# Kernel tuning notes

Measured on AMD Instinct MI355X. Metric: run time of the kernel, lower is better.

## Reference

```python
import jax, jax.numpy as jnp
import numpy as np

EMBED_DIM = 1024
NUM_HEADS = 16
HEAD_DIM = EMBED_DIM // NUM_HEADS


def setup_inputs() -> dict:
    key = jax.random.key(0)
    k1, k2, k3, k4 = jax.random.split(key, 4)
    S, B = 2048, 2
    x = jax.random.normal(k1, (S, B, EMBED_DIM), dtype=jnp.float32)
    # xavier_uniform for in_proj_weight [3E, E]
    limit_in = float(np.sqrt(6.0 / (3 * EMBED_DIM + EMBED_DIM)))
    in_proj_weight = jax.random.uniform(k2, (3 * EMBED_DIM, EMBED_DIM), minval=-limit_in, maxval=limit_in, dtype=jnp.float32)
    in_proj_bias = jnp.zeros((3 * EMBED_DIM,), dtype=jnp.float32)
    # out_proj: nn.Linear default init (kaiming-uniform-ish); use uniform of similar scale
    limit_out = float(np.sqrt(1.0 / EMBED_DIM))
    out_proj_weight = jax.random.uniform(k3, (EMBED_DIM, EMBED_DIM), minval=-limit_out, maxval=limit_out, dtype=jnp.float32)
    out_proj_bias = jnp.zeros((EMBED_DIM,), dtype=jnp.float32)
    return {
        "x": x,
        "in_proj_weight": in_proj_weight,
        "in_proj_bias": in_proj_bias,
        "out_proj_weight": out_proj_weight,
        "out_proj_bias": out_proj_bias,
    }


def reference(x, in_proj_weight, in_proj_bias, out_proj_weight, out_proj_bias):
    S, B, E = x.shape
    H, D = NUM_HEADS, HEAD_DIM
    scaling = float(D) ** -0.5
    # fused QKV projection: [S, B, 3E]
    qkv = jnp.einsum("sbe,fe->sbf", x, in_proj_weight) + in_proj_bias
    q, k, v = jnp.split(qkv, 3, axis=-1)
    q = q * scaling
    # [S, B, E] -> [B*H, S, D]
    def to_heads(t):
        return t.reshape(S, B * H, D).transpose(1, 0, 2)
    q, k, v = to_heads(q), to_heads(k), to_heads(v)
    # attention scores [B*H, S, S]
    scores = jnp.einsum("btd,bsd->bts", q, k)
    weights = jax.nn.softmax(scores, axis=-1)
    # dropout p=0.0 -> identity
    attn = jnp.einsum("bts,bsd->btd", weights, v)  # [B*H, S, D]
    attn = attn.transpose(1, 0, 2).reshape(S, B, E)
    out = jnp.einsum("sbe,fe->sbf", attn, out_proj_weight) + out_proj_bias
    return out
```

## Files before the change

### kernel.cpp

```cpp
#include <hip/hip_runtime.h>

typedef __bf16 bf16_t;
typedef __attribute__((ext_vector_type(8))) __bf16 bf16x8;
typedef __attribute__((ext_vector_type(4))) __bf16 bf16x4;
typedef __attribute__((ext_vector_type(4))) float f32x4;
typedef __attribute__((ext_vector_type(16))) float f32x16;
typedef __attribute__((ext_vector_type(2))) unsigned uint2v;

#define MFMA16(a, b, c) __builtin_amdgcn_mfma_f32_16x16x32_bf16((a), (b), (c), 0, 0, 0)
#define MFMA32(a, b, c) __builtin_amdgcn_mfma_f32_32x32x16_bf16((a), (b), (c), 0, 0, 0)
#define LOG2E 1.44269504088896f

__device__ __forceinline__ void async16(const bf16_t* g, bf16_t* l) {
    __builtin_amdgcn_global_load_lds(
        (const __attribute__((address_space(1))) unsigned int*)g,
        (__attribute__((address_space(3))) unsigned int*)l, 16, 0, 0);
}

__device__ __forceinline__ unsigned pack2(float a, float b) {
    union { bf16_t e[2]; unsigned u; } x;
    x.e[0] = (bf16_t)a; x.e[1] = (bf16_t)b;
    return x.u;
}

__device__ __forceinline__ void pl32swap(unsigned& a, unsigned& b) {
    uint2v r = __builtin_amdgcn_permlane32_swap(a, b, false, false);
    a = r[0]; b = r[1];
}

__global__ __launch_bounds__(256) void conv3(
    const float* __restrict__ s0, const float* __restrict__ s1,
    const float* __restrict__ s2, bf16_t* __restrict__ dst,
    int n0, int n1)
{
    const int i = (blockIdx.x * 256 + threadIdx.x) * 8;
    const float* src;
    int off;
    if (i < n0)           { src = s0; off = 0; }
    else if (i < n0 + n1) { src = s1; off = n0; }
    else                  { src = s2; off = n0 + n1; }
    const float4 a = *reinterpret_cast<const float4*>(src + i - off);
    const float4 b = *reinterpret_cast<const float4*>(src + i - off + 4);
    bf16x8 o;
    o[0] = (bf16_t)a.x; o[1] = (bf16_t)a.y; o[2] = (bf16_t)a.z; o[3] = (bf16_t)a.w;
    o[4] = (bf16_t)b.x; o[5] = (bf16_t)b.y; o[6] = (bf16_t)b.z; o[7] = (bf16_t)b.w;
    *reinterpret_cast<bf16x8*>(dst + i) = o;
}

__global__ __launch_bounds__(256) void vtrans(
    const bf16_t* __restrict__ qkv, bf16_t* __restrict__ vT, int B)
{
    const int bh = blockIdx.x, b = bh >> 4, h = bh & 15;
    const int s0 = blockIdx.y * 64;
    __shared__ bf16_t Ls[64][65];
    const int t = threadIdx.x;
    const int sl = t & 63, dc = t >> 6;
#pragma unroll
    for (int pass = 0; pass < 2; pass++) {
        const int d8 = dc + pass * 4;
        bf16x8 v = *reinterpret_cast<const bf16x8*>(
            qkv + (size_t)((s0 + sl) * B + b) * 3072 + 2048 + h * 64 + d8 * 8);
#pragma unroll
        for (int j = 0; j < 8; j++) Ls[sl][d8 * 8 + j] = v[j];
    }
    __syncthreads();
#pragma unroll
    for (int pass = 0; pass < 2; pass++) {
        const int cid = t + pass * 256;
        const int d = cid >> 3, cs = cid & 7;
        bf16x8 o;
#pragma unroll
        for (int j = 0; j < 8; j++) o[j] = Ls[cs * 8 + j][d];
        *reinterpret_cast<bf16x8*>(
            vT + (size_t)(bh * 64 + d) * 2048 + s0 + cs * 8) = o;
    }
}

template <int MT, bool F32OUT>
__global__ __launch_bounds__(256, 3) void gemm_nt_lds(
    const bf16_t* __restrict__ W, const bf16_t* __restrict__ X,
    const float* __restrict__ bias, void* __restrict__ Cv,
    int N, int K, int scale_lim, float qscale, int fpx)
{
    constexpr int NJ = MT / 32;
    __shared__ bf16_t As[2][128 * 32];
    __shared__ bf16_t Bs[2][MT * 32];

    const int lane = threadIdx.x & 63;
    const int wv   = threadIdx.x >> 6;
    const int l15  = lane & 15;
    const int qd   = lane >> 4;

    const int id = blockIdx.x;
    const int x8 = id & 7, k = id >> 3;
    const int fb = ((k % fpx) * 8 + x8) * 128;
    const int mb = (k / fpx) * MT;
    const int fw = (wv & 1) * 64;
    const int mw = (wv >> 1) * (MT / 2);

    f32x4 acc[4][NJ] = {};

    auto stage = [&](int set, int k0) {
#pragma unroll
        for (int t = 0; t < 2; t++) {
            const int p = (wv * 2 + t) * 64 + lane;
            const int r = p >> 2, cl = (p & 3) ^ (r & 3);
            async16(W + (size_t)(fb + r) * K + k0 + cl * 8,
                    &As[set][(wv * 2 + t) * 512]);
        }
#pragma unroll
        for (int t = 0; t < MT / 64; t++) {
            const int p = (wv * (MT / 64) + t) * 64 + lane;
            const int r = p >> 2, cl = (p & 3) ^ (r & 3);
            async16(X + (size_t)(mb + r) * K + k0 + cl * 8,
                    &Bs[set][(wv * (MT / 64) + t) * 512]);
        }
    };

    stage(0, 0);
    int set = 0;
    for (int k0 = 0; k0 < K; k0 += 32) {
        __syncthreads();
        if (k0 + 32 < K) stage(set ^ 1, k0 + 32);

        const int s3 = l15 & 3;
        bf16x8 a[4], bb[NJ];
#pragma unroll
        for (int i = 0; i < 4; i++)
            a[i] = *reinterpret_cast<const bf16x8*>(
                &As[set][(fw + i * 16 + l15) * 32 + ((qd ^ s3) * 8)]);
#pragma unroll
        for (int j = 0; j < NJ; j++)
            bb[j] = *reinterpret_cast<const bf16x8*>(
                &Bs[set][(mw + j * 16 + l15) * 32 + ((qd ^ s3) * 8)]);
#pragma unroll
        for (int i = 0; i < 4; i++)
#pragma unroll
            for (int j = 0; j < NJ; j++)
                acc[i][j] = MFMA16(a[i], bb[j], acc[i][j]);
        set ^= 1;
    }

    const float scale = (fb < scale_lim) ? qscale : 1.0f;
#pragma unroll
    for (int i = 0; i < 4; i++) {
        const int f0 = fb + fw + i * 16 + qd * 4;
        float bs[4];
#pragma unroll
        for (int r = 0; r < 4; r++) bs[r] = bias[f0 + r];
#pragma unroll
        for (int j = 0; j < NJ; j++) {
            const int m = mb + mw + j * 16 + l15;
            if (F32OUT) {
                float4 o;
                o.x = (acc[i][j][0] + bs[0]) * scale;
                o.y = (acc[i][j][1] + bs[1]) * scale;
                o.z = (acc[i][j][2] + bs[2]) * scale;
                o.w = (acc[i][j][3] + bs[3]) * scale;
                *reinterpret_cast<float4*>((float*)Cv + (size_t)m * N + f0) = o;
            } else {
                bf16x4 o;
#pragma unroll
                for (int r = 0; r < 4; r++)
                    o[r] = (bf16_t)((acc[i][j][r] + bs[r]) * scale);
                *reinterpret_cast<bf16x4*>((bf16_t*)Cv + (size_t)m * N + f0) = o;
            }
        }
    }
}

__global__ __launch_bounds__(256, 2) void flash_attn(
    const bf16_t* __restrict__ qkv, const bf16_t* __restrict__ vT,
    bf16_t* __restrict__ attn, int S, int B)
{
    const int E3 = 3072, E = 1024;
    const int bh = blockIdx.x, b = bh >> 4, h = bh & 15;
    const int tid = threadIdx.x, lane = tid & 63, wv = tid >> 6;
    const int qw = wv & 1;
    const int pr = wv >> 1;
    const int l31 = lane & 31, half = lane >> 5;

    __shared__ bf16_t Kt[2][2][64 * 64];
    __shared__ bf16_t Vt[2][2][64 * 64];
    __shared__ float  lsh[2][64];

    const int q0 = blockIdx.y * 128 + qw * 64;

    bf16x8 qf[2][4];
#pragma unroll
    for (int qt = 0; qt < 2; qt++) {
        const bf16_t* qp = qkv + (size_t)((q0 + qt * 32 + l31) * B + b) * E3 + h * 64;
#pragma unroll
        for (int ks = 0; ks < 4; ks++)
            qf[qt][ks] = *reinterpret_cast<const bf16x8*>(qp + ks * 16 + half * 8);
    }

    f32x16 oacc[2][2] = {};
    float lrun[2] = {0.0f, 0.0f};

    auto stage = [&](int set, int kv) {
#pragma unroll
        for (int t = 0; t < 4; t++) {
            const int p = (qw * 4 + t) * 64 + lane;
            const int r = p >> 3, cl = (p & 7) ^ (r & 7);
            async16(qkv + (size_t)((kv + r) * B + b) * E3 + E + h * 64 + cl * 8,
                    &Kt[pr][set][(qw * 4 + t) * 512]);
            async16(vT + (size_t)(bh * 64 + r) * 2048 + kv + cl * 8,
                    &Vt[pr][set][(qw * 4 + t) * 512]);
        }
    };

    const int kvbase = pr * (S / 2);
    const int NIT = S / 128;

    stage(0, kvbase);
    int set = 0;
    for (int it = 0; it < NIT; it++) {
        __syncthreads();
        if (it + 1 < NIT) stage(set ^ 1, kvbase + (it + 1) * 64);

        const bf16_t* K_ = Kt[pr][set];
        const bf16_t* V_ = Vt[pr][set];

        union PF { unsigned u[4]; bf16x8 v; };
        PF pf[2][4];
#pragma unroll
        for (int nt = 0; nt < 2; nt++) {
            const int r = nt * 32 + l31;
            const int r7 = r & 7;
            bf16x8 kf[4];
#pragma unroll
            for (int ks = 0; ks < 4; ks++)
                kf[ks] = *reinterpret_cast<const bf16x8*>(
                    K_ + r * 64 + (((ks * 2 + half) ^ r7) * 8));
#pragma unroll
            for (int qt = 0; qt < 2; qt++) {
                f32x16 st = {};
                __builtin_amdgcn_s_setprio(1);
#pragma unroll
                for (int ks = 0; ks < 4; ks++)
                    st = MFMA32(kf[ks], qf[qt][ks], st);
                __builtin_amdgcn_s_setprio(0);
                float ls = 0.0f;
                unsigned q8[8];
#pragma unroll
                for (int g = 0; g < 4; g++) {
                    const float p0 = __builtin_amdgcn_exp2f(st[4 * g]);
                    const float p1 = __builtin_amdgcn_exp2f(st[4 * g + 1]);
                    const float p2 = __builtin_amdgcn_exp2f(st[4 * g + 2]);
                    const float p3 = __builtin_amdgcn_exp2f(st[4 * g + 3]);
                    ls += (p0 + p1) + (p2 + p3);
                    q8[2 * g]     = pack2(p0, p1);
                    q8[2 * g + 1] = pack2(p2, p3);
                }
                lrun[qt] += ls;
                pl32swap(q8[0], q8[2]); pl32swap(q8[1], q8[3]);
                pl32swap(q8[4], q8[6]); pl32swap(q8[5], q8[7]);
                pf[qt][nt * 2 + 0].u[0] = q8[0]; pf[qt][nt * 2 + 0].u[1] = q8[1];
                pf[qt][nt * 2 + 0].u[2] = q8[2]; pf[qt][nt * 2 + 0].u[3] = q8[3];
                pf[qt][nt * 2 + 1].u[0] = q8[4]; pf[qt][nt * 2 + 1].u[1] = q8[5];
                pf[qt][nt * 2 + 1].u[2] = q8[6]; pf[qt][nt * 2 + 1].u[3] = q8[7];
            }
        }
        __builtin_amdgcn_s_setprio(1);
#pragma unroll
        for (int kn = 0; kn < 4; kn++)
#pragma unroll
            for (int dt = 0; dt < 2; dt++) {
                const int d = dt * 32 + l31;
                bf16x8 vf = *reinterpret_cast<const bf16x8*>(
                    V_ + d * 64 + (((kn * 2 + half) ^ (d & 7)) * 8));
                oacc[0][dt] = MFMA32(vf, pf[0][kn].v, oacc[0][dt]);
                oacc[1][dt] = MFMA32(vf, pf[1][kn].v, oacc[1][dt]);
            }
        __builtin_amdgcn_s_setprio(0);
        set ^= 1;
    }

    __syncthreads();
    float lr[2];
#pragma unroll
    for (int qt = 0; qt < 2; qt++) lr[qt] = lrun[qt] + __shfl_xor(lrun[qt], 32);

    float* fo = reinterpret_cast<float*>(&Kt[0][0][0]) + qw * 4096;

    if (pr == 1) {
#pragma unroll
        for (int qt = 0; qt < 2; qt++) {
            const int ql = qt * 32 + l31;
            lsh[qw][ql] = lr[qt];
#pragma unroll
            for (int dt = 0; dt < 2; dt++)
#pragma unroll
                for (int g = 0; g < 4; g++)
#pragma unroll
                    for (int r = 0; r < 4; r++) {
                        const int d = dt * 32 + g * 8 + half * 4 + r;
                        fo[d * 64 + ql] = oacc[qt][dt][4 * g + r];
                    }
        }
    }
    __syncthreads();
    if (pr == 0) {
#pragma unroll
        for (int qt = 0; qt < 2; qt++) {
            const int ql = qt * 32 + l31;
            const float inv = 1.0f / (lr[qt] + lsh[qw][ql]);
            const int qrow = q0 + qt * 32 + l31;
#pragma unroll
            for (int dt = 0; dt < 2; dt++)
#pragma unroll
                for (int g = 0; g < 4; g++) {
                    bf16x4 o;
#pragma unroll
                    for (int r = 0; r < 4; r++) {
                        const int d = dt * 32 + g * 8 + half * 4 + r;
                        o[r] = (bf16_t)((oacc[qt][dt][4 * g + r] + fo[d * 64 + ql]) * inv);
                    }
                    *reinterpret_cast<bf16x4*>(attn + (size_t)(qrow * B + b) * E +
                                               h * 64 + dt * 32 + g * 8 + half * 4) = o;
                }
        }
    }
}

extern "C" void kernel_launch(void* const* d_in, const int* in_sizes, int n_in,
                              void* d_out, int out_size, void* d_ws, size_t ws_size,
                              hipStream_t stream) {
    const float* x  = (const float*)d_in[0];
    const float* wi = (const float*)d_in[1];
    const float* bi = (const float*)d_in[2];
    const float* wo = (const float*)d_in[3];
    const float* bo = (const float*)d_in[4];
    float* out = (float*)d_out;

    const int S = 2048, B = 2, E = 1024;
    const int M = S * B;

    bf16_t* xb   = (bf16_t*)d_ws;
    bf16_t* wib  = xb  + (size_t)M * E;
    bf16_t* wob  = wib + (size_t)3 * E * E;
    bf16_t* qkv  = wob + (size_t)E * E;
    bf16_t* attn = qkv + (size_t)M * 3 * E;
    bf16_t* vT   = xb;

    const int n0 = M * E, n1 = 3 * E * E, n2 = E * E;
    conv3<<<(n0 + n1 + n2) / 8 / 256, 256, 0, stream>>>(x, wi, wo, xb, n0, n1);

    gemm_nt_lds<128, false><<<(3 * E / 128) * (M / 128), 256, 0, stream>>>(
        wib, xb, bi, qkv, 3 * E, E, E, 0.125f * LOG2E, (3 * E / 128) / 8);

    vtrans<<<dim3(B * 16, S / 64), 256, 0, stream>>>(qkv, vT, B);

    flash_attn<<<dim3(B * 16, S / 128), 256, 0, stream>>>(qkv, vT, attn, S, B);

    gemm_nt_lds<64, true><<<(E / 128) * (M / 64), 256, 0, stream>>>(
        wob, attn, bo, out, E, E, 0, 1.0f, (E / 128) / 8);
}
```

Measured before the change: 194.1 us.

## Software-pipeline attention loop, overlapping previous tile's PV MFMAs with current QK softmax

Restructures the flash-attention inner loop so the P·V product for the previous KV tile is interleaved with the Q·K MFMAs and exp2 softmax of the current tile. P fragments are double-buffered in registers (pfA/pfB), and V staging is delayed by one iteration with its own buffer indexing. A final epilogue does the last tile's PV after the loop. The aim is to hide exp/pack latency behind MFMA work, at the cost of higher register pressure and more complex buffer indexing.

```diff
diff --git a/kernel.cpp b/kernel.cpp
--- a/kernel.cpp
+++ b/kernel.cpp
@@ -198,32 +198,30 @@
     f32x16 oacc[2][2] = {};
     float lrun[2] = {0.0f, 0.0f};
 
-    auto stage = [&](int set, int kv) {
+    auto stageK = [&](int kset, int kv) {
 #pragma unroll
         for (int t = 0; t < 4; t++) {
             const int p = (qw * 4 + t) * 64 + lane;
             const int r = p >> 3, cl = (p & 7) ^ (r & 7);
             async16(qkv + (size_t)((kv + r) * B + b) * E3 + E + h * 64 + cl * 8,
-                    &Kt[pr][set][(qw * 4 + t) * 512]);
+                    &Kt[pr][kset][(qw * 4 + t) * 512]);
+        }
+    };
+    auto stageV = [&](int vset, int kv) {
+#pragma unroll
+        for (int t = 0; t < 4; t++) {
+            const int p = (qw * 4 + t) * 64 + lane;
+            const int r = p >> 3, cl = (p & 7) ^ (r & 7);
             async16(vT + (size_t)(bh * 64 + r) * 2048 + kv + cl * 8,
-                    &Vt[pr][set][(qw * 4 + t) * 512]);
+                    &Vt[pr][vset][(qw * 4 + t) * 512]);
         }
     };
 
-    const int kvbase = pr * (S / 2);
-    const int NIT = S / 128;
-
-    stage(0, kvbase);
-    int set = 0;
-    for (int it = 0; it < NIT; it++) {
-        __syncthreads();
-        if (it + 1 < NIT) stage(set ^ 1, kvbase + (it + 1) * 64);
-
-        const bf16_t* K_ = Kt[pr][set];
-        const bf16_t* V_ = Vt[pr][set];
-
-        union PF { unsigned u[4]; bf16x8 v; };
-        PF pf[2][4];
+    union PF { unsigned u[4]; bf16x8 v; };
+    PF pfA[2][4], pfB[2][4];
+
+    auto body = [&](PF (&pw)[2][4], PF (&prd)[2][4],
+                    const bf16_t* K_, const bf16_t* Vp, bool doPV) {
 #pragma unroll
         for (int nt = 0; nt < 2; nt++) {
             const int r = nt * 32 + l31;
@@ -240,6 +238,17 @@
 #pragma unroll
                 for (int ks = 0; ks < 4; ks++)
                     st = MFMA32(kf[ks], qf[qt][ks], st);
+                if (doPV) {
+                    const int kn = nt * 2 + qt;
+#pragma unroll
+                    for (int dt = 0; dt < 2; dt++) {
+                        const int d = dt * 32 + l31;
+                        bf16x8 vf = *reinterpret_cast<const bf16x8*>(
+                            Vp + d * 64 + (((kn * 2 + half) ^ (d & 7)) * 8));
+                        oacc[0][dt] = MFMA32(vf, prd[0][kn].v, oacc[0][dt]);
+                        oacc[1][dt] = MFMA32(vf, prd[1][kn].v, oacc[1][dt]);
+                    }
+                }
                 __builtin_amdgcn_s_setprio(0);
                 float ls = 0.0f;
                 unsigned q8[8];
@@ -256,12 +265,36 @@
                 lrun[qt] += ls;
                 pl32swap(q8[0], q8[2]); pl32swap(q8[1], q8[3]);
                 pl32swap(q8[4], q8[6]); pl32swap(q8[5], q8[7]);
-                pf[qt][nt * 2 + 0].u[0] = q8[0]; pf[qt][nt * 2 + 0].u[1] = q8[1];
-                pf[qt][nt * 2 + 0].u[2] = q8[2]; pf[qt][nt * 2 + 0].u[3] = q8[3];
-                pf[qt][nt * 2 + 1].u[0] = q8[4]; pf[qt][nt * 2 + 1].u[1] = q8[5];
-                pf[qt][nt * 2 + 1].u[2] = q8[6]; pf[qt][nt * 2 + 1].u[3] = q8[7];
+                pw[qt][nt * 2 + 0].u[0] = q8[0]; pw[qt][nt * 2 + 0].u[1] = q8[1];
+                pw[qt][nt * 2 + 0].u[2] = q8[2]; pw[qt][nt * 2 + 0].u[3] = q8[3];
+                pw[qt][nt * 2 + 1].u[0] = q8[4]; pw[qt][nt * 2 + 1].u[1] = q8[5];
+                pw[qt][nt * 2 + 1].u[2] = q8[6]; pw[qt][nt * 2 + 1].u[3] = q8[7];
             }
         }
+    };
+
+    const int kvbase = pr * (S / 2);
+    const int NIT = S / 128;
+
+    stageK(0, kvbase);
+    stageV(0, kvbase);
+    int set = 0;
+    for (int it = 0; it < NIT; it++) {
+        __syncthreads();
+        if (it + 1 < NIT) stageK(set ^ 1, kvbase + (it + 1) * 64);
+        if (it > 0)       stageV(it & 1, kvbase + it * 64);
+
+        const bf16_t* K_ = Kt[pr][set];
+        const bf16_t* Vp = Vt[pr][(it & 1) ^ 1];
+        if (it & 1) body(pfB, pfA, K_, Vp, it > 0);
+        else        body(pfA, pfB, K_, Vp, it > 0);
+        set ^= 1;
+    }
+
+    __syncthreads();
+    {
+        const bf16_t* Vp = Vt[pr][(NIT - 1) & 1];
+        PF (&prd)[2][4] = ((NIT - 1) & 1) ? pfB : pfA;
         __builtin_amdgcn_s_setprio(1);
 #pragma unroll
         for (int kn = 0; kn < 4; kn++)
@@ -269,15 +302,13 @@
             for (int dt = 0; dt < 2; dt++) {
                 const int d = dt * 32 + l31;
                 bf16x8 vf = *reinterpret_cast<const bf16x8*>(
-                    V_ + d * 64 + (((kn * 2 + half) ^ (d & 7)) * 8));
-                oacc[0][dt] = MFMA32(vf, pf[0][kn].v, oacc[0][dt]);
-                oacc[1][dt] = MFMA32(vf, pf[1][kn].v, oacc[1][dt]);
+                    Vp + d * 64 + (((kn * 2 + half) ^ (d & 7)) * 8));
+                oacc[0][dt] = MFMA32(vf, prd[0][kn].v, oacc[0][dt]);
+                oacc[1][dt] = MFMA32(vf, prd[1][kn].v, oacc[1][dt]);
             }
         __builtin_amdgcn_s_setprio(0);
-        set ^= 1;
-    }
-
-    __syncthreads();
+    }
+
     float lr[2];
 #pragma unroll
     for (int qt = 0; qt < 2; qt++) lr[qt] = lrun[qt] + __shfl_xor(lrun[qt], 32);
```

Measured after the change: 392.9 us. +102.4%, slower.
